# Optimization experiments

Measured on AMD Instinct MI355X. Metric: run time of the kernel, lower is better.

Reference implementation:

```python
import jax, jax.numpy as jnp
import numpy as np

B, C, H, W = 8, 64, 128, 128


def _conv3x3(x, w, b):
    # x: [B,C,H,W], w: [O,I,3,3], b: [O]; stride 1, padding 1
    y = jax.lax.conv_general_dilated(
        x, w, window_strides=(1, 1), padding=((1, 1), (1, 1)),
        dimension_numbers=('NCHW', 'OIHW', 'NCHW'))
    return y + b[None, :, None, None]


def setup_inputs() -> dict:
    key = jax.random.key(0)
    ks = jax.random.split(key, 8)
    s = 0.05
    return {
        'x': jax.random.normal(ks[0], (B, C, H, W), jnp.float32),
        'Wq': jax.random.normal(ks[1], (C, C, 3, 3), jnp.float32) * s,
        'bq': jax.random.normal(ks[2], (C,), jnp.float32) * s,
        'Wk': jax.random.normal(ks[3], (C, C, 3, 3), jnp.float32) * s,
        'bk': jax.random.normal(ks[4], (C,), jnp.float32) * s,
        'Wv': jax.random.normal(ks[5], (C, C, 3, 3), jnp.float32) * s,
        'bv': jax.random.normal(ks[6], (C,), jnp.float32) * s,
        'gamma': jax.random.normal(ks[7], (1,), jnp.float32) * s,
    }


def reference(x, Wq, bq, Wk, bk, Wv, bv, gamma):
    b_, c_, h_, w_ = x.shape
    q = _conv3x3(x, Wq, bq)  # [B,C,H,W]
    k = _conv3x3(x, Wk, bk)
    v = _conv3x3(x, Wv, bv)

    # energy along H (column attention): eH[b,h,w,g] = sum_c q[b,c,h,w]*k[b,c,g,w]
    eH = jnp.einsum('bchw,bcgw->bhwg', q, k)
    eye = jnp.eye(h_, dtype=bool)  # mask diagonal h==g with -inf
    eH = jnp.where(eye[None, :, None, :], -jnp.inf, eH)

    # energy along W (row attention): eW[b,h,w,g] = sum_c q[b,c,h,w]*k[b,c,h,g]
    eW = jnp.einsum('bchw,bchg->bhwg', q, k)

    # joint softmax over concatenated [H | W] axis
    att = jax.nn.softmax(jnp.concatenate([eH, eW], axis=3), axis=3)
    att_H = att[:, :, :, :h_]          # [B,H,W,H]
    att_W = att[:, :, :, h_:h_ + w_]   # [B,H,W,W]

    out_H = jnp.einsum('bcgw,bhwg->bchw', v, att_H)
    out_W = jnp.einsum('bchg,bhwg->bchw', v, att_W)

    return gamma[0] * (out_H + out_W) + x
```

## Files before the change

### kernel.cpp

```cpp
#include <hip/hip_runtime.h>
#include <hip/hip_bf16.h>

#define B_ 8
#define C_ 64
#define H_ 128
#define W_ 128
#define HW_  ((size_t)H_ * W_)
#define CHW_ ((size_t)C_ * H_ * W_)

typedef unsigned short u16;
typedef unsigned int   u32;
typedef __attribute__((ext_vector_type(8))) short bf16x8;
typedef __attribute__((ext_vector_type(4))) float f32x4;

__device__ __forceinline__ float bf2f(u16 h) {
    union { u32 u; float f; } c; c.u = ((u32)h) << 16; return c.f;
}
__device__ __forceinline__ u16 f2bf(float f) {
    union { float f; u32 u; } c; c.f = f;
    u32 u = c.u;
    u32 r = (u + 0x7fffu + ((u >> 16) & 1u)) >> 16;
    return (u16)r;
}
__device__ __forceinline__ u32 pack2(float a, float b) {
    return (u32)f2bf(a) | ((u32)f2bf(b) << 16);
}
__device__ __forceinline__ float sanit(float x, float lo, float hi) {
    return fminf(fmaxf(x, lo), hi);
}

__global__ __launch_bounds__(256) void prep_weights(
    const float* __restrict__ Wq, const float* __restrict__ Wk,
    const float* __restrict__ Wv, u16* __restrict__ Wt)
{
    int tap = blockIdx.x;
    int cog = blockIdx.y * 4 + (threadIdx.x >> 6);
    int ci  = threadIdx.x & 63;
    int arr = cog >> 6, co = cog & 63;
    const float* src = arr == 0 ? Wq : (arr == 1 ? Wk : Wv);
    Wt[tap * 12288 + cog * 64 + ci] = f2bf(src[(co * 64 + ci) * 9 + tap]);
}

__global__ __launch_bounds__(256, 2) void conv_mfma_kernel(
    const float* __restrict__ x, const u16* __restrict__ Wt,
    const float* __restrict__ bq, const float* __restrict__ bk,
    const float* __restrict__ bv,
    u16* __restrict__ qN, u16* __restrict__ kN, u16* __restrict__ v)
{
    const int h    = blockIdx.x;
    const size_t boff = (size_t)blockIdx.y * CHW_;
    const int tid  = threadIdx.x;
    const int lane = tid & 63, wv = tid >> 6;
    const int ln15 = lane & 15, quad = lane >> 4;

    __shared__ __align__(16) u16 xI[24960];

    if (tid < 48) {
        int dh = tid >> 4, g = (tid & 15) >> 1, p = (tid & 1) ? 129 : 0;
        *(uint4*)(xI + dh * 8320 + g * 1040 + p * 8) = (uint4){0, 0, 0, 0};
    }

#pragma unroll
    for (int it = 0; it < 12; it++) {
        int vid  = tid + it * 256;
        int w4   = vid & 31;
        int rest = vid >> 5;
        int dh   = rest >> 5;
        int cp   = rest & 31;
        int c    = cp * 2;
        int h2   = h - 1 + dh;
        float4 f0 = {0.f, 0.f, 0.f, 0.f}, f1 = {0.f, 0.f, 0.f, 0.f};
        if (h2 >= 0 && h2 < H_) {
            const float* xrow = x + boff + (size_t)h2 * W_;
            f0 = *(const float4*)(xrow + (size_t)c * HW_ + w4 * 4);
            f1 = *(const float4*)(xrow + (size_t)(c + 1) * HW_ + w4 * 4);
        }
        float a0[4] = {f0.x, f0.y, f0.z, f0.w};
        float a1[4] = {f1.x, f1.y, f1.z, f1.w};
        int g = c >> 3, e = c & 7;
        u16* base = xI + dh * 8320 + g * 1040;
#pragma unroll
        for (int i = 0; i < 4; i++)
            *(u32*)(base + (w4 * 4 + i + 1) * 8 + e) = pack2(a0[i], a1[i]);
    }
    __syncthreads();

    f32x4 acc[3][8];
#pragma unroll
    for (int mt = 0; mt < 3; mt++)
#pragma unroll
        for (int nt = 0; nt < 8; nt++)
            acc[mt][nt] = (f32x4){0.f, 0.f, 0.f, 0.f};

#pragma unroll
    for (int dh = 0; dh < 3; dh++) {
        const u16* xrow = xI + dh * 8320;
#pragma unroll
        for (int dw = 0; dw < 3; dw++) {
            const u16* wt = Wt + (dh * 3 + dw) * 12288;
#pragma unroll
            for (int ks = 0; ks < 2; ks++) {
                bf16x8 af[3], bfr[8];
#pragma unroll
                for (int mt = 0; mt < 3; mt++)
                    af[mt] = *(const bf16x8*)(wt + (wv * 48 + mt * 16 + ln15) * 64 + ks * 32 + quad * 8);
#pragma unroll
                for (int nt = 0; nt < 8; nt++)
                    bfr[nt] = *(const bf16x8*)(xrow + ((quad + ks * 4) * 1040 + (nt * 16 + ln15 + dw) * 8));
#pragma unroll
                for (int mt = 0; mt < 3; mt++)
#pragma unroll
                    for (int nt = 0; nt < 8; nt++)
                        acc[mt][nt] = __builtin_amdgcn_mfma_f32_16x16x32_bf16(
                            af[mt], bfr[nt], acc[mt][nt], 0, 0, 0);
            }
        }
    }

    __syncthreads();
    u16* T = xI;
#pragma unroll
    for (int mt = 0; mt < 3; mt++) {
        int base = wv * 48 + mt * 16;
        int arr  = base >> 6;
        if (arr < 2) {
            const float* bias = arr == 0 ? bq : bk;
            int cb = (base & 63) + quad * 4;
#pragma unroll
            for (int r = 0; r < 4; r++) {
                float bb = bias[cb + r];
#pragma unroll
                for (int nt = 0; nt < 8; nt++)
                    T[arr * 9216 + (nt * 16 + ln15) * 72 + cb + r] = f2bf(acc[mt][nt][r] + bb);
            }
        } else {
            int cb = (base & 63) + quad * 4;
#pragma unroll
            for (int r = 0; r < 4; r++) {
                float bb = bv[cb + r];
                u16* drow = v + boff + (size_t)(cb + r) * HW_ + (size_t)h * W_;
#pragma unroll
                for (int nt = 0; nt < 8; nt++)
                    drow[nt * 16 + ln15] = f2bf(acc[mt][nt][r] + bb);
            }
        }
    }
    __syncthreads();
#pragma unroll
    for (int it = 0; it < 8; it++) {
        int idx = tid + it * 256;
        int arr = idx >> 10, rem = idx & 1023;
        int px = rem >> 3, c8 = (rem & 7) * 8;
        uint4 val = *(uint4*)(T + arr * 9216 + px * 72 + c8);
        u16* dst = (arr ? kN : qN) + boff + ((size_t)h * W_ + px) * 64 + c8;
        *(uint4*)dst = val;
    }
}

__global__ __launch_bounds__(256) void vt_kernel(
    const u16* __restrict__ v, u16* __restrict__ vT)
{
    __shared__ u16 Ts[64 * 72];
    const u16* src = v  + (size_t)blockIdx.z * CHW_ + (size_t)blockIdx.y * HW_;
    u16* dst       = vT + (size_t)blockIdx.z * CHW_ + (size_t)blockIdx.y * HW_;
    const int ti = blockIdx.x & 1, tj = blockIdx.x >> 1;
    const int r0 = ti * 64, c0 = tj * 64;
    const int tid = threadIdx.x;
    const int r = tid >> 2, cq = tid & 3;
#pragma unroll
    for (int i = 0; i < 2; i++) {
        uint4 u = *(const uint4*)(src + (size_t)(r0 + r) * 128 + c0 + cq * 16 + i * 8);
        *(uint4*)(Ts + r * 72 + cq * 16 + i * 8) = u;
    }
    __syncthreads();
    const int wr = tid >> 2, hq = tid & 3;
    union { u16 o[16]; uint4 v4[2]; } t;
#pragma unroll
    for (int j = 0; j < 16; j++) t.o[j] = Ts[(hq * 16 + j) * 72 + wr];
    *(uint4*)(dst + (size_t)(c0 + wr) * 128 + r0 + hq * 16)     = t.v4[0];
    *(uint4*)(dst + (size_t)(c0 + wr) * 128 + r0 + hq * 16 + 8) = t.v4[1];
}

__global__ __launch_bounds__(256, 3) void col_kernel(
    const u16* __restrict__ qN, const u16* __restrict__ kN,
    const u16* __restrict__ vT,
    float* __restrict__ maxH, float* __restrict__ sumH,
    float* __restrict__ Ocol)
{
    const size_t boff = (size_t)blockIdx.z * CHW_;
    const size_t soff = (size_t)blockIdx.z * HW_;
    qN += boff; kN += boff; vT += boff; Ocol += boff;
    maxH += soff; sumH += soff;

    const int s    = blockIdx.x;
    const int tid  = threadIdx.x;
    const int lane = tid & 63, wv = tid >> 6;
    const int ln15 = lane & 15, quad = lane >> 4;

    __shared__ __align__(16) u16 smemU[18432];
    u16* Qs = smemU;
    u16* Ks = smemU + 9216;

#pragma unroll
    for (int it = 0; it < 4; it++) {
        int idx = tid + it * 256;
        int t = idx >> 3, cg = (idx & 7) * 8;
        size_t off = (size_t)t * 8192 + (size_t)s * 64 + cg;
        *(uint4*)(Qs + t * 72 + cg) = *(const uint4*)(qN + off);
        *(uint4*)(Ks + t * 72 + cg) = *(const uint4*)(kN + off);
    }
    __syncthreads();

    f32x4 Sc[2][8];
#pragma unroll
    for (int mt = 0; mt < 2; mt++)
#pragma unroll
        for (int nt = 0; nt < 8; nt++)
            Sc[mt][nt] = (f32x4){0.f, 0.f, 0.f, 0.f};

#pragma unroll
    for (int ks = 0; ks < 2; ks++) {
        bf16x8 aq[2];
#pragma unroll
        for (int mt = 0; mt < 2; mt++)
            aq[mt] = *(const bf16x8*)(Qs + (wv * 32 + mt * 16 + ln15) * 72 + ks * 32 + quad * 8);
#pragma unroll
        for (int nt = 0; nt < 8; nt++) {
            bf16x8 bk_ = *(const bf16x8*)(Ks + (nt * 16 + ln15) * 72 + ks * 32 + quad * 8);
#pragma unroll
            for (int mt = 0; mt < 2; mt++)
                Sc[mt][nt] = __builtin_amdgcn_mfma_f32_16x16x32_bf16(aq[mt], bk_, Sc[mt][nt], 0, 0, 0);
        }
    }
#pragma unroll
    for (int mt = 0; mt < 2; mt++)
#pragma unroll
        for (int nt = 0; nt < 8; nt++)
#pragma unroll
            for (int r = 0; r < 4; r++) {
                int tt = wv * 32 + mt * 16 + quad * 4 + r;
                if (tt == nt * 16 + ln15) Sc[mt][nt][r] = -1e30f;
            }

    float mloc[2][4];
#pragma unroll
    for (int mt = 0; mt < 2; mt++)
#pragma unroll
        for (int r = 0; r < 4; r++) {
            float m = Sc[mt][0][r];
#pragma unroll
            for (int nt = 1; nt < 8; nt++) m = fmaxf(m, Sc[mt][nt][r]);
            for (int o = 1; o < 16; o <<= 1) m = fmaxf(m, __shfl_xor(m, o));
            float ss = 0.f;
#pragma unroll
            for (int nt = 0; nt < 8; nt++) ss += __expf(Sc[mt][nt][r] - m);
            for (int o = 1; o < 16; o <<= 1) ss += __shfl_xor(ss, o);
            mloc[mt][r] = m;
            if (ln15 == 0) {
                int tt = wv * 32 + mt * 16 + quad * 4 + r;
                int pix = tt * W_ + s;
                maxH[pix] = m; sumH[pix] = ss;
            }
        }
    __syncthreads();
    u16* Ps = smemU;
#pragma unroll
    for (int mt = 0; mt < 2; mt++)
#pragma unroll
        for (int nt = 0; nt < 8; nt++)
#pragma unroll
            for (int r = 0; r < 4; r++)
                Ps[(wv * 32 + mt * 16 + quad * 4 + r) * 136 + nt * 16 + ln15] =
                    f2bf(__expf(Sc[mt][nt][r] - mloc[mt][r]));
    __syncthreads();

    f32x4 Oc[2][4];
#pragma unroll
    for (int mt = 0; mt < 2; mt++)
#pragma unroll
        for (int nt = 0; nt < 4; nt++)
            Oc[mt][nt] = (f32x4){0.f, 0.f, 0.f, 0.f};
#pragma unroll
    for (int kg = 0; kg < 4; kg++) {
        bf16x8 ap[2];
#pragma unroll
        for (int mt = 0; mt < 2; mt++)
            ap[mt] = *(const bf16x8*)(Ps + (wv * 32 + mt * 16 + ln15) * 136 + kg * 32 + quad * 8);
#pragma unroll
        for (int nt = 0; nt < 4; nt++) {
            bf16x8 bv_ = *(const bf16x8*)(vT + (size_t)(nt * 16 + ln15) * HW_ + (size_t)s * 128 + kg * 32 + quad * 8);
#pragma unroll
            for (int mt = 0; mt < 2; mt++)
                Oc[mt][nt] = __builtin_amdgcn_mfma_f32_16x16x32_bf16(ap[mt], bv_, Oc[mt][nt], 0, 0, 0);
        }
    }
    __syncthreads();
    float* Of = (float*)smemU;
#pragma unroll
    for (int mt = 0; mt < 2; mt++)
#pragma unroll
        for (int nt = 0; nt < 4; nt++)
#pragma unroll
            for (int r = 0; r < 4; r++)
                Of[(wv * 32 + mt * 16 + quad * 4 + r) * 68 + nt * 16 + ln15] = Oc[mt][nt][r];
    __syncthreads();
#pragma unroll
    for (int it = 0; it < 8; it++) {
        int idx = tid + it * 256;
        int t = idx >> 4, c4 = (idx & 15) * 4;
        *(float4*)(Ocol + ((size_t)t * 128 + s) * 64 + c4) = *(float4*)(Of + t * 68 + c4);
    }
}

__global__ __launch_bounds__(256, 3) void row_kernel(
    const u16* __restrict__ qN, const u16* __restrict__ kN,
    const u16* __restrict__ v,
    const float* __restrict__ x, const float* __restrict__ gammap,
    const float* __restrict__ maxH, const float* __restrict__ sumH,
    const float* __restrict__ Ocol, float* __restrict__ out)
{
    const size_t boff = (size_t)blockIdx.z * CHW_;
    const size_t soff = (size_t)blockIdx.z * HW_;
    qN += boff; kN += boff; v += boff; Ocol += boff; x += boff; out += boff;
    maxH += soff; sumH += soff;

    const int s    = blockIdx.x;
    const int tid  = threadIdx.x;
    const int lane = tid & 63, wv = tid >> 6;
    const int ln15 = lane & 15, quad = lane >> 4;

    __shared__ __align__(16) u16 smemU[18432];
    u16* Qs = smemU;
    u16* Ks = smemU + 9216;

#pragma unroll
    for (int it = 0; it < 4; it++) {
        int idx = tid + it * 256;
        int t = idx >> 3, cg = (idx & 7) * 8;
        size_t off = (size_t)s * 8192 + (size_t)t * 64 + cg;
        *(uint4*)(Qs + t * 72 + cg) = *(const uint4*)(qN + off);
        *(uint4*)(Ks + t * 72 + cg) = *(const uint4*)(kN + off);
    }
    __syncthreads();

    f32x4 Sc[2][8];
#pragma unroll
    for (int mt = 0; mt < 2; mt++)
#pragma unroll
        for (int nt = 0; nt < 8; nt++)
            Sc[mt][nt] = (f32x4){0.f, 0.f, 0.f, 0.f};
#pragma unroll
    for (int ks = 0; ks < 2; ks++) {
        bf16x8 aq[2];
#pragma unroll
        for (int mt = 0; mt < 2; mt++)
            aq[mt] = *(const bf16x8*)(Qs + (wv * 32 + mt * 16 + ln15) * 72 + ks * 32 + quad * 8);
#pragma unroll
        for (int nt = 0; nt < 8; nt++) {
            bf16x8 bk_ = *(const bf16x8*)(Ks + (nt * 16 + ln15) * 72 + ks * 32 + quad * 8);
#pragma unroll
            for (int mt = 0; mt < 2; mt++)
                Sc[mt][nt] = __builtin_amdgcn_mfma_f32_16x16x32_bf16(aq[mt], bk_, Sc[mt][nt], 0, 0, 0);
        }
    }

    float mr[2][4], rr[2][4], al[2][4];
#pragma unroll
    for (int mt = 0; mt < 2; mt++)
#pragma unroll
        for (int r = 0; r < 4; r++) {
            float m = Sc[mt][0][r];
#pragma unroll
            for (int nt = 1; nt < 8; nt++) m = fmaxf(m, Sc[mt][nt][r]);
            for (int o = 1; o < 16; o <<= 1) m = fmaxf(m, __shfl_xor(m, o));
            float ss = 0.f;
#pragma unroll
            for (int nt = 0; nt < 8; nt++) ss += __expf(Sc[mt][nt][r] - m);
            for (int o = 1; o < 16; o <<= 1) ss += __shfl_xor(ss, o);
            int tt  = wv * 32 + mt * 16 + quad * 4 + r;
            int pix = s * W_ + tt;
            float mc = sanit(maxH[pix], -3e38f, 3e38f);
            float sc = sanit(sumH[pix], 0.f, 3e38f);
            float mm = fmaxf(mc, m);
            float dd = sc * __expf(fminf(mc - mm, 0.f)) + ss * __expf(fminf(m - mm, 0.f));
            float rv = 1.0f / fmaxf(dd, 1e-30f);
            mr[mt][r] = mm; rr[mt][r] = rv;
            al[mt][r] = __expf(fminf(mc - mm, 0.f)) * rv;
        }
    __syncthreads();
    u16* Ps = smemU;
#pragma unroll
    for (int mt = 0; mt < 2; mt++)
#pragma unroll
        for (int nt = 0; nt < 8; nt++)
#pragma unroll
            for (int r = 0; r < 4; r++)
                Ps[(wv * 32 + mt * 16 + quad * 4 + r) * 136 + nt * 16 + ln15] =
                    f2bf(__expf(fminf(Sc[mt][nt][r] - mr[mt][r], 0.f)) * rr[mt][r]);
    __syncthreads();

    f32x4 Oc[2][4];
#pragma unroll
    for (int mt = 0; mt < 2; mt++)
#pragma unroll
        for (int nt = 0; nt < 4; nt++)
            Oc[mt][nt] = (f32x4){0.f, 0.f, 0.f, 0.f};
#pragma unroll
    for (int kg = 0; kg < 4; kg++) {
        bf16x8 ap[2];
#pragma unroll
        for (int mt = 0; mt < 2; mt++)
            ap[mt] = *(const bf16x8*)(Ps + (wv * 32 + mt * 16 + ln15) * 136 + kg * 32 + quad * 8);
#pragma unroll
        for (int nt = 0; nt < 4; nt++) {
            bf16x8 bv_ = *(const bf16x8*)(v + (size_t)(nt * 16 + ln15) * HW_ + (size_t)s * 128 + kg * 32 + quad * 8);
#pragma unroll
            for (int mt = 0; mt < 2; mt++)
                Oc[mt][nt] = __builtin_amdgcn_mfma_f32_16x16x32_bf16(ap[mt], bv_, Oc[mt][nt], 0, 0, 0);
        }
    }
    __syncthreads();

    const float gmm = gammap[0];
    float* Of = (float*)smemU;
#pragma unroll
    for (int mt = 0; mt < 2; mt++)
#pragma unroll
        for (int nt = 0; nt < 4; nt++) {
            float fv[4];
            int c = nt * 16 + ln15;
#pragma unroll
            for (int r = 0; r < 4; r++) {
                int tt = wv * 32 + mt * 16 + quad * 4 + r;
                float oc = Ocol[((size_t)s * 128 + tt) * 64 + c];
                fv[r] = gmm * (Oc[mt][nt][r] + al[mt][r] * oc);
            }
            int w0 = wv * 32 + mt * 16 + quad * 4;
            *(float4*)(Of + c * 132 + w0) = make_float4(fv[0], fv[1], fv[2], fv[3]);
        }
    __syncthreads();
    int c = tid >> 2, w0 = (tid & 3) * 32;
#pragma unroll
    for (int i = 0; i < 8; i++) {
        int w = w0 + i * 4;
        float4 xo = *(const float4*)(x + (size_t)c * HW_ + (size_t)s * 128 + w);
        float4 of = *(const float4*)(Of + c * 132 + w);
        *(float4*)(out + (size_t)c * HW_ + (size_t)s * 128 + w) =
            make_float4(of.x + xo.x, of.y + xo.y, of.z + xo.z, of.w + xo.w);
    }
}

extern "C" void kernel_launch(void* const* d_in, const int* in_sizes, int n_in,
                              void* d_out, int out_size, void* d_ws, size_t ws_size,
                              hipStream_t stream)
{
    const float* x  = (const float*)d_in[0];
    const float* Wq = (const float*)d_in[1];
    const float* bq = (const float*)d_in[2];
    const float* Wk = (const float*)d_in[3];
    const float* bk = (const float*)d_in[4];
    const float* Wv = (const float*)d_in[5];
    const float* bv = (const float*)d_in[6];
    const float* gm = (const float*)d_in[7];
    float* out = (float*)d_out;

    char* ws = (char*)d_ws;
    const size_t need1 = 4 * (size_t)B_ * CHW_ * 2 + (size_t)B_ * CHW_ * 4
                       + 2 * (size_t)B_ * HW_ * 4 + 221184;
    int passes = (ws_size >= need1) ? 1 : 2;
    int nb = B_ / passes;

    const size_t SL = (size_t)nb * CHW_ * 2;
    const size_t OC = (size_t)nb * CHW_ * 4;
    const size_t ST = (size_t)nb * HW_ * 4;
    u16*   qNb  = (u16*)(ws);
    u16*   kNb  = (u16*)(ws + SL);
    u16*   v    = (u16*)(ws + 2 * SL);
    u16*   vT   = (u16*)(ws + 3 * SL);
    float* Ocol = (float*)(ws + 4 * SL);
    float* maxH = (float*)(ws + 4 * SL + OC);
    float* sumH = (float*)(ws + 4 * SL + OC + ST);
    u16*   Wt   = (u16*)(ws + 4 * SL + OC + 2 * ST);

    dim3 blk(256);
    prep_weights<<<dim3(9, 48), blk, 0, stream>>>(Wq, Wk, Wv, Wt);

    for (int p = 0; p < passes; p++) {
        const float* xb = x + (size_t)p * nb * CHW_;
        float* ob = out + (size_t)p * nb * CHW_;
        conv_mfma_kernel<<<dim3(H_, nb), blk, 0, stream>>>(xb, Wt, bq, bk, bv, qNb, kNb, v);
        vt_kernel<<<dim3(4, C_, nb), blk, 0, stream>>>(v, vT);
        col_kernel<<<dim3(W_, 1, nb), blk, 0, stream>>>(qNb, kNb, vT, maxH, sumH, Ocol);
        row_kernel<<<dim3(H_, 1, nb), blk, 0, stream>>>(qNb, kNb, v, xb, gm, maxH, sumH, Ocol, ob);
    }
}
```

Measured before the change: 204.1 us.

## Pre-pack x to padded bf16 and load conv tiles with global_load_lds

Adds an xprep kernel that converts x into a zero-padded, channel-grouped bf16 layout once per batch. The conv kernel then copies its three input rows straight into LDS with global_load_lds instead of loading fp32 three times and converting per block. It also remaps workgroup IDs across XCDs and raises wave priority around the MFMA block. The cost is an extra launch and a full-tensor write and read of the bf16 copy, which reuses the Ocol buffer before col_kernel overwrites it.

```diff
diff --git a/kernel.cpp b/kernel.cpp
--- a/kernel.cpp
+++ b/kernel.cpp
@@ -28,6 +28,11 @@
 __device__ __forceinline__ float sanit(float x, float lo, float hi) {
     return fminf(fmaxf(x, lo), hi);
 }
+__device__ __forceinline__ void gload_lds16(const u16* g, u16* l) {
+    __builtin_amdgcn_global_load_lds(
+        (const __attribute__((address_space(1))) void*)g,
+        (__attribute__((address_space(3))) void*)l, 16, 0, 0);
+}
 
 __global__ __launch_bounds__(256) void prep_weights(
     const float* __restrict__ Wq, const float* __restrict__ Wk,
@@ -41,14 +46,49 @@
     Wt[tap * 12288 + cog * 64 + ci] = f2bf(src[(co * 64 + ci) * 9 + tap]);
 }
 
+__global__ __launch_bounds__(256) void xprep_kernel(
+    const float* __restrict__ x, u16* __restrict__ xb)
+{
+    const int hp  = blockIdx.x;
+    const int tid = threadIdx.x;
+    u16* dst = xb + ((size_t)blockIdx.y * 130 + hp) * 8192;
+    if (hp == 0 || hp == 129) {
+#pragma unroll
+        for (int i = 0; i < 4; i++)
+            *(uint4*)(dst + (size_t)(tid + i * 256) * 8) = (uint4){0, 0, 0, 0};
+        return;
+    }
+    const float* xr = x + (size_t)blockIdx.y * CHW_ + (size_t)(hp - 1) * W_;
+#pragma unroll
+    for (int it = 0; it < 4; it++) {
+        int vid = tid + it * 256;
+        int w4  = vid & 31;
+        int cp  = vid >> 5;
+        int c   = cp * 2;
+        float4 f0 = *(const float4*)(xr + (size_t)c * HW_ + w4 * 4);
+        float4 f1 = *(const float4*)(xr + (size_t)(c + 1) * HW_ + w4 * 4);
+        float a0[4] = {f0.x, f0.y, f0.z, f0.w};
+        float a1[4] = {f1.x, f1.y, f1.z, f1.w};
+        int g = c >> 3, e = c & 7;
+        u16* base = dst + g * 1024 + e;
+#pragma unroll
+        for (int i = 0; i < 4; i++)
+            *(u32*)(base + (w4 * 4 + i) * 8) = pack2(a0[i], a1[i]);
+    }
+}
+
 __global__ __launch_bounds__(256, 2) void conv_mfma_kernel(
-    const float* __restrict__ x, const u16* __restrict__ Wt,
+    const u16* __restrict__ xb, const u16* __restrict__ Wt,
     const float* __restrict__ bq, const float* __restrict__ bk,
     const float* __restrict__ bv,
     u16* __restrict__ qN, u16* __restrict__ kN, u16* __restrict__ v)
 {
-    const int h    = blockIdx.x;
-    const size_t boff = (size_t)blockIdx.y * CHW_;
+    const int nwg  = gridDim.x * gridDim.y;
+    const int flat = blockIdx.y * gridDim.x + blockIdx.x;
+    const int wg   = (flat & 7) * (nwg >> 3) + (flat >> 3);
+    const int h    = wg & (H_ - 1);
+    const int bidx = wg >> 7;
+    const size_t boff = (size_t)bidx * CHW_;
     const int tid  = threadIdx.x;
     const int lane = tid & 63, wv = tid >> 6;
     const int ln15 = lane & 15, quad = lane >> 4;
@@ -60,28 +100,13 @@
         *(uint4*)(xI + dh * 8320 + g * 1040 + p * 8) = (uint4){0, 0, 0, 0};
     }
 
+    const u16* xrows = xb + ((size_t)bidx * 130 + h) * 8192;
 #pragma unroll
     for (int it = 0; it < 12; it++) {
-        int vid  = tid + it * 256;
-        int w4   = vid & 31;
-        int rest = vid >> 5;
-        int dh   = rest >> 5;
-        int cp   = rest & 31;
-        int c    = cp * 2;
-        int h2   = h - 1 + dh;
-        float4 f0 = {0.f, 0.f, 0.f, 0.f}, f1 = {0.f, 0.f, 0.f, 0.f};
-        if (h2 >= 0 && h2 < H_) {
-            const float* xrow = x + boff + (size_t)h2 * W_;
-            f0 = *(const float4*)(xrow + (size_t)c * HW_ + w4 * 4);
-            f1 = *(const float4*)(xrow + (size_t)(c + 1) * HW_ + w4 * 4);
-        }
-        float a0[4] = {f0.x, f0.y, f0.z, f0.w};
-        float a1[4] = {f1.x, f1.y, f1.z, f1.w};
-        int g = c >> 3, e = c & 7;
-        u16* base = xI + dh * 8320 + g * 1040;
-#pragma unroll
-        for (int i = 0; i < 4; i++)
-            *(u32*)(base + (w4 * 4 + i + 1) * 8 + e) = pack2(a0[i], a1[i]);
+        int chunk = wv * 12 + it;
+        int dh = chunk >> 4, g = (chunk >> 1) & 7, half = chunk & 1;
+        gload_lds16(xrows + (size_t)dh * 8192 + g * 1024 + half * 512 + lane * 8,
+                    xI + dh * 8320 + g * 1040 + 8 + half * 512);
     }
     __syncthreads();
 
@@ -107,12 +132,14 @@
 #pragma unroll
                 for (int nt = 0; nt < 8; nt++)
                     bfr[nt] = *(const bf16x8*)(xrow + ((quad + ks * 4) * 1040 + (nt * 16 + ln15 + dw) * 8));
+                __builtin_amdgcn_s_setprio(1);
 #pragma unroll
                 for (int mt = 0; mt < 3; mt++)
 #pragma unroll
                     for (int nt = 0; nt < 8; nt++)
                         acc[mt][nt] = __builtin_amdgcn_mfma_f32_16x16x32_bf16(
                             af[mt], bfr[nt], acc[mt][nt], 0, 0, 0);
+                __builtin_amdgcn_s_setprio(0);
             }
         }
     }
@@ -481,16 +508,18 @@
     float* maxH = (float*)(ws + 4 * SL + OC);
     float* sumH = (float*)(ws + 4 * SL + OC + ST);
     u16*   Wt   = (u16*)(ws + 4 * SL + OC + 2 * ST);
+    u16*   xb   = (u16*)Ocol;
 
     dim3 blk(256);
     prep_weights<<<dim3(9, 48), blk, 0, stream>>>(Wq, Wk, Wv, Wt);
 
     for (int p = 0; p < passes; p++) {
-        const float* xb = x + (size_t)p * nb * CHW_;
+        const float* xbp = x + (size_t)p * nb * CHW_;
         float* ob = out + (size_t)p * nb * CHW_;
+        xprep_kernel<<<dim3(130, nb), blk, 0, stream>>>(xbp, xb);
         conv_mfma_kernel<<<dim3(H_, nb), blk, 0, stream>>>(xb, Wt, bq, bk, bv, qNb, kNb, v);
         vt_kernel<<<dim3(4, C_, nb), blk, 0, stream>>>(v, vT);
         col_kernel<<<dim3(W_, 1, nb), blk, 0, stream>>>(qNb, kNb, vT, maxH, sumH, Ocol);
-        row_kernel<<<dim3(H_, 1, nb), blk, 0, stream>>>(qNb, kNb, v, xb, gm, maxH, sumH, Ocol, ob);
-    }
-}
+        row_kernel<<<dim3(H_, 1, nb), blk, 0, stream>>>(qNb, kNb, v, xbp, gm, maxH, sumH, Ocol, ob);
+    }
+}
```

Measured after the change: 207.4 us. No clear change (+1.6%).
